# Kernel tuning notes

Hardware: AMD Instinct MI355X
Metric: run time of the kernel (lower is better)

The kernel has to match this reference:

```python
import jax, jax.numpy as jnp
import numpy as np

N = 262144      # active coordinates
M = 131072      # rulebook entries per kernel offset
C_IN = 64
C_OUT = 64


def setup_inputs() -> dict:
    key = jax.random.key(0)
    k1, k2, k3, k4 = jax.random.split(key, 4)
    coords = jax.random.randint(k1, (N, 3), 0, 512, dtype=jnp.int64) if jax.config.jax_enable_x64 else jax.random.randint(k1, (N, 3), 0, 512, dtype=jnp.int32)
    feats = jax.random.normal(k2, (N, C_IN), dtype=jnp.float32)
    in_rows = jax.random.randint(k3, (9, M), 0, N, dtype=jnp.int32)
    out_rows = jax.random.randint(k4, (9, M), 0, N, dtype=jnp.int32)
    # weight init matches torch: randn * (1/sqrt(in_ch))
    weight = jax.random.normal(jax.random.fold_in(key, 5), (9, C_IN, C_OUT), dtype=jnp.float32) * (1.0 / C_IN ** 0.5)
    bias = jnp.zeros((C_OUT,), dtype=jnp.float32)
    return {"coords": coords, "feats": feats, "in_rows": in_rows,
            "out_rows": out_rows, "weight": weight, "bias": bias}


def reference(coords, feats, in_rows, out_rows, weight, bias):
    # Gather input features for all 9 kernel offsets: [9, M, C_in]
    gathered = feats[in_rows]
    # Per-offset GEMM: [9, M, C_out]
    prod = jnp.einsum('kmi,kio->kmo', gathered, weight)
    # Scatter-add into output rows
    out = jnp.zeros((feats.shape[0], weight.shape[2]), dtype=feats.dtype)
    out = out.at[out_rows.reshape(-1)].add(prod.reshape(-1, weight.shape[2]))
    out = out + bias
    return (coords, out)
```

## Files before the change

### kernel.cpp

```cpp
#include <hip/hip_runtime.h>
#include <hip/hip_bf16.h>

#define NPTS 262144
#define MRB  131072
#define KOFF 9
#define NENT (KOFF * MRB)

typedef __attribute__((ext_vector_type(8))) short short8;
typedef __attribute__((ext_vector_type(4))) short short4v;
typedef __attribute__((ext_vector_type(4))) float f32x4;

__device__ __forceinline__ short f2bf(float f) {
    __hip_bfloat16 h = __float2bfloat16(f);
    return __builtin_bit_cast(short, h);
}
__device__ __forceinline__ float bf2f(unsigned short u) {
    unsigned int x = ((unsigned int)u) << 16;
    return __builtin_bit_cast(float, x);
}
__device__ __forceinline__ void atomic_add_f32(float* p, float v) {
    __hip_atomic_fetch_add(p, v, __ATOMIC_RELAXED, __HIP_MEMORY_SCOPE_AGENT);
}

#define PROD_OFF   0ull
#define POS_OFF    150994944ull
#define START_OFF  155713536ull
#define CURSOR_OFF 156762368ull
#define COUNTS_OFF 157810944ull
#define BSUM_OFF   158859520ull
#define WS_NEED    158860544ull


__global__ __launch_bounds__(256) void init_fast(const int* __restrict__ coords,
                                                 float* __restrict__ out,
                                                 int* __restrict__ counts) {
    const int i = blockIdx.x * 256 + threadIdx.x;
    const int nc4 = (NPTS * 3) / 4;
    if (i < nc4) {
        int4 c = ((const int4*)coords)[i];
        float4 f;
        f.x = (float)c.x; f.y = (float)c.y; f.z = (float)c.z; f.w = (float)c.w;
        ((float4*)out)[i] = f;
    } else {
        int j = i - nc4;
        ((int4*)counts)[j] = make_int4(0, 0, 0, 0);
    }
}

__global__ __launch_bounds__(256) void hist_kernel(const int* __restrict__ out_rows,
                                                   int* __restrict__ counts) {
    const int e = blockIdx.x * 256 + threadIdx.x;
    atomicAdd(&counts[out_rows[e]], 1);
}

__global__ __launch_bounds__(1024) void scan_blocks(const int* __restrict__ counts,
                                                    int* __restrict__ start,
                                                    int* __restrict__ bsum) {
    __shared__ int lds[1024];
    const int tid = threadIdx.x;
    const int gid = blockIdx.x * 1024 + tid;
    int v = counts[gid];
    lds[tid] = v;
    __syncthreads();
#pragma unroll
    for (int off = 1; off < 1024; off <<= 1) {
        int t = (tid >= off) ? lds[tid - off] : 0;
        __syncthreads();
        lds[tid] += t;
        __syncthreads();
    }
    start[gid] = lds[tid] - v;
    if (tid == 1023) bsum[blockIdx.x] = lds[tid];
}

__global__ __launch_bounds__(256) void scan_bsum(int* __restrict__ bsum) {
    __shared__ int lds[256];
    const int tid = threadIdx.x;
    int v = bsum[tid];
    lds[tid] = v;
    __syncthreads();
#pragma unroll
    for (int off = 1; off < 256; off <<= 1) {
        int t = (tid >= off) ? lds[tid - off] : 0;
        __syncthreads();
        lds[tid] += t;
        __syncthreads();
    }
    bsum[tid] = lds[tid] - v;
}

__global__ __launch_bounds__(1024) void add_offsets(int* __restrict__ start,
                                                    const int* __restrict__ bsum,
                                                    int* __restrict__ cursor) {
    const int gid = blockIdx.x * 1024 + threadIdx.x;
    int s = start[gid] + bsum[blockIdx.x];
    start[gid] = s;
    cursor[gid] = s;
    if (gid == 0) start[NPTS] = NENT;
}

__global__ __launch_bounds__(256) void fill_pos(const int* __restrict__ out_rows,
                                                int* __restrict__ cursor,
                                                int* __restrict__ pos) {
    const int e = blockIdx.x * 256 + threadIdx.x;
    pos[e] = atomicAdd(&cursor[out_rows[e]], 1);
}

__global__ __launch_bounds__(256) void conv_prod(const float* __restrict__ feats,
                                                 const int*   __restrict__ in_rows,
                                                 const float* __restrict__ weight,
                                                 const int*   __restrict__ pos,
                                                 short*       __restrict__ prod) {
    const int lane = threadIdx.x & 63;
    const int wv   = threadIdx.x >> 6;
    const int lrow = lane & 15;
    const int lhi  = lane >> 4;
    const int BPK  = MRB / 64;
    const int k    = blockIdx.x / BPK;
    const int mb   = (blockIdx.x % BPK) * 64 + wv * 16;

    const float* Wk = weight + k * 64 * 64;
    short8 wfrag[2][4];
#pragma unroll
    for (int kk = 0; kk < 2; ++kk)
#pragma unroll
        for (int mt = 0; mt < 4; ++mt)
#pragma unroll
            for (int j = 0; j < 8; ++j)
                wfrag[kk][mt][j] = f2bf(Wk[(kk * 32 + lhi * 8 + j) * 64 + mt * 16 + lrow]);

    const int e    = k * MRB + mb + lrow;
    const int arow = in_rows[e];
    const float* ap = feats + (long)arow * 64 + lhi * 8;

    f32x4 acc[4] = {};
#pragma unroll
    for (int kk = 0; kk < 2; ++kk) {
        float4 f0 = *(const float4*)(ap + kk * 32);
        float4 f1 = *(const float4*)(ap + kk * 32 + 4);
        short8 ffrag;
        ffrag[0] = f2bf(f0.x); ffrag[1] = f2bf(f0.y);
        ffrag[2] = f2bf(f0.z); ffrag[3] = f2bf(f0.w);
        ffrag[4] = f2bf(f1.x); ffrag[5] = f2bf(f1.y);
        ffrag[6] = f2bf(f1.z); ffrag[7] = f2bf(f1.w);
#pragma unroll
        for (int mt = 0; mt < 4; ++mt)
            acc[mt] = __builtin_amdgcn_mfma_f32_16x16x32_bf16(wfrag[kk][mt], ffrag, acc[mt], 0, 0, 0);
    }

    const int p = pos[e];
    short* pp = prod + (size_t)p * 64 + lhi * 4;
#pragma unroll
    for (int mt = 0; mt < 4; ++mt) {
        short4v s;
        s[0] = f2bf(acc[mt][0]); s[1] = f2bf(acc[mt][1]);
        s[2] = f2bf(acc[mt][2]); s[3] = f2bf(acc[mt][3]);
        *(short4v*)(pp + mt * 16) = s;
    }
}

__global__ __launch_bounds__(256) void reduce_out(const short* __restrict__ prod,
                                                  const int*   __restrict__ start,
                                                  const float* __restrict__ bias,
                                                  float*       __restrict__ out) {
    const int lane = threadIdx.x & 63;
    const int wid  = (blockIdx.x * 256 + threadIdx.x) >> 6;
    const int nw   = (gridDim.x * 256) >> 6;
    const float b  = bias[lane];
    for (int r = wid; r < NPTS; r += nw) {
        const int s0 = start[r], s1 = start[r + 1];
        float acc = 0.f;
        const unsigned short* p = (const unsigned short*)prod + (size_t)s0 * 64 + lane;
        for (int s = s0; s < s1; ++s, p += 64)
            acc += bf2f(*p);
        out[(size_t)r * 64 + lane] = acc + b;
    }
}

__global__ __launch_bounds__(256) void init_full(const int* __restrict__ coords,
                                                 const float* __restrict__ bias,
                                                 float* __restrict__ out) {
    const int tid = blockIdx.x * blockDim.x + threadIdx.x;
    const int nc4 = (NPTS * 3) / 4;
    const int nf4 = (NPTS * 64) / 4;
    for (int i = tid; i < nc4 + nf4; i += gridDim.x * blockDim.x) {
        if (i < nc4) {
            int4 c = ((const int4*)coords)[i];
            float4 f;
            f.x = (float)c.x; f.y = (float)c.y; f.z = (float)c.z; f.w = (float)c.w;
            ((float4*)out)[i] = f;
        } else {
            int j = i - nc4;
            float4 b = ((const float4*)bias)[j & 15];
            ((float4*)(out + (size_t)NPTS * 3))[j] = b;
        }
    }
}

__global__ __launch_bounds__(256) void conv_atomic(const float* __restrict__ feats,
                                                   const int*   __restrict__ in_rows,
                                                   const int*   __restrict__ out_rows,
                                                   const float* __restrict__ weight,
                                                   float*       __restrict__ out) {
    const int lane = threadIdx.x & 63;
    const int wv   = threadIdx.x >> 6;
    const int lrow = lane & 15;
    const int lhi  = lane >> 4;
    const int BPK  = MRB / 64;
    const int k    = blockIdx.x / BPK;
    const int mb   = (blockIdx.x % BPK) * 64 + wv * 16;

    const float* Wk = weight + k * 64 * 64;
    short8 bfrag[2][4];
#pragma unroll
    for (int kk = 0; kk < 2; ++kk)
#pragma unroll
        for (int nt = 0; nt < 4; ++nt)
#pragma unroll
            for (int j = 0; j < 8; ++j)
                bfrag[kk][nt][j] = f2bf(Wk[(kk * 32 + lhi * 8 + j) * 64 + nt * 16 + lrow]);

    const int arow = in_rows[k * MRB + mb + lrow];
    const float* ap = feats + (long)arow * 64 + lhi * 8;

    f32x4 acc[4] = {};
#pragma unroll
    for (int kk = 0; kk < 2; ++kk) {
        float4 f0 = *(const float4*)(ap + kk * 32);
        float4 f1 = *(const float4*)(ap + kk * 32 + 4);
        short8 afrag;
        afrag[0] = f2bf(f0.x); afrag[1] = f2bf(f0.y);
        afrag[2] = f2bf(f0.z); afrag[3] = f2bf(f0.w);
        afrag[4] = f2bf(f1.x); afrag[5] = f2bf(f1.y);
        afrag[6] = f2bf(f1.z); afrag[7] = f2bf(f1.w);
#pragma unroll
        for (int nt = 0; nt < 4; ++nt)
            acc[nt] = __builtin_amdgcn_mfma_f32_16x16x32_bf16(afrag, bfrag[kk][nt], acc[nt], 0, 0, 0);
    }

    const int ob = k * MRB + mb + lhi * 4;
#pragma unroll
    for (int r = 0; r < 4; ++r) {
        const int orow = out_rows[ob + r];
        float* op = out + (long)orow * 64 + lrow;
#pragma unroll
        for (int nt = 0; nt < 4; ++nt)
            atomic_add_f32(op + nt * 16, acc[nt][r]);
    }
}

extern "C" void kernel_launch(void* const* d_in, const int* in_sizes, int n_in,
                              void* d_out, int out_size, void* d_ws, size_t ws_size,
                              hipStream_t stream) {
    const int*   coords   = (const int*)  d_in[0];
    const float* feats    = (const float*)d_in[1];
    const int*   in_rows  = (const int*)  d_in[2];
    const int*   out_rows = (const int*)  d_in[3];
    const float* weight   = (const float*)d_in[4];
    const float* bias     = (const float*)d_in[5];
    float* out      = (float*)d_out;
    float* out_feat = out + (size_t)NPTS * 3;

    if (ws_size >= WS_NEED) {
        char* ws = (char*)d_ws;
        short* prod  = (short*)(ws + PROD_OFF);
        int* pos     = (int*)(ws + POS_OFF);
        int* start   = (int*)(ws + START_OFF);
        int* cursor  = (int*)(ws + CURSOR_OFF);
        int* counts  = (int*)(ws + COUNTS_OFF);
        int* bsum    = (int*)(ws + BSUM_OFF);

        hipLaunchKernelGGL(init_fast,   dim3(1024), dim3(256),  0, stream, coords, out, counts);
        hipLaunchKernelGGL(hist_kernel, dim3(NENT / 256), dim3(256), 0, stream, out_rows, counts);
        hipLaunchKernelGGL(scan_blocks, dim3(NPTS / 1024), dim3(1024), 0, stream, counts, start, bsum);
        hipLaunchKernelGGL(scan_bsum,   dim3(1),    dim3(256),  0, stream, bsum);
        hipLaunchKernelGGL(add_offsets, dim3(NPTS / 1024), dim3(1024), 0, stream, start, bsum, cursor);
        hipLaunchKernelGGL(fill_pos,    dim3(NENT / 256), dim3(256), 0, stream, out_rows, cursor, pos);
        hipLaunchKernelGGL(conv_prod,   dim3(KOFF * (MRB / 64)), dim3(256), 0, stream,
                           feats, in_rows, weight, pos, prod);
        hipLaunchKernelGGL(reduce_out,  dim3(2048), dim3(256),  0, stream, prod, start, bias, out_feat);
    } else {
        hipLaunchKernelGGL(init_full,  dim3(2048), dim3(256), 0, stream, coords, bias, out);
        hipLaunchKernelGGL(conv_atomic, dim3(KOFF * (MRB / 64)), dim3(256), 0, stream,
                           feats, in_rows, out_rows, weight, out_feat);
    }
}
```

Measured before the change: 439.8 us.

## Pre-convert feats and weights to bf16, write prod in entry order, gather via index

A prep kernel now converts feats to bf16 and pre-swizzles weights into MFMA fragment layout once, so conv_prod reads half the gathered bytes and skips per-block weight conversion. conv_prod writes products contiguously by entry instead of scattering to sorted positions, and fill_idx records a sorted index list instead. reduce_out then gathers products through that index with four rows in flight per wave and reduces with shuffles. The cost is an extra feats pass, extra workspace, and indirect, less coalesced reads in the reduction.

```diff
diff --git a/kernel.cpp b/kernel.cpp
--- a/kernel.cpp
+++ b/kernel.cpp
@@ -22,28 +22,56 @@
     __hip_atomic_fetch_add(p, v, __ATOMIC_RELAXED, __HIP_MEMORY_SCOPE_AGENT);
 }
 
-#define PROD_OFF   0ull
-#define POS_OFF    150994944ull
-#define START_OFF  155713536ull
-#define CURSOR_OFF 156762368ull
-#define COUNTS_OFF 157810944ull
-#define BSUM_OFF   158859520ull
-#define WS_NEED    158860544ull
-
-
-__global__ __launch_bounds__(256) void init_fast(const int* __restrict__ coords,
-                                                 float* __restrict__ out,
-                                                 int* __restrict__ counts) {
-    const int i = blockIdx.x * 256 + threadIdx.x;
-    const int nc4 = (NPTS * 3) / 4;
-    if (i < nc4) {
-        int4 c = ((const int4*)coords)[i];
-        float4 f;
-        f.x = (float)c.x; f.y = (float)c.y; f.z = (float)c.z; f.w = (float)c.w;
-        ((float4*)out)[i] = f;
-    } else {
-        int j = i - nc4;
-        ((int4*)counts)[j] = make_int4(0, 0, 0, 0);
+#define FB_OFF     0ull
+#define WBF_OFF    33554432ull
+#define PROD_OFF   33628160ull
+#define IDX_OFF    184623104ull
+#define START_OFF  189341696ull
+#define CURSOR_OFF 190390528ull
+#define COUNTS_OFF 191439104ull
+#define BSUM_OFF   192487680ull
+#define WS_NEED    192488704ull
+
+
+__global__ __launch_bounds__(256) void prep(const int*   __restrict__ coords,
+                                            const float* __restrict__ feats,
+                                            const float* __restrict__ weight,
+                                            float* __restrict__ out,
+                                            int*   __restrict__ counts,
+                                            short* __restrict__ fb,
+                                            short* __restrict__ wbf) {
+    const int T0 = (NPTS * 3) / 4;
+    const int T1 = T0 + NPTS / 4;
+    const int T2 = T1 + NPTS * 16;
+    const int T3 = T2 + (KOFF * 8 * 64);
+    const int stride = gridDim.x * 256;
+    for (int i = blockIdx.x * 256 + threadIdx.x; i < T3; i += stride) {
+        if (i < T0) {
+            int4 c = ((const int4*)coords)[i];
+            float4 f;
+            f.x = (float)c.x; f.y = (float)c.y; f.z = (float)c.z; f.w = (float)c.w;
+            ((float4*)out)[i] = f;
+        } else if (i < T1) {
+            ((int4*)counts)[i - T0] = make_int4(0, 0, 0, 0);
+        } else if (i < T2) {
+            int j = i - T1;
+            float4 f = ((const float4*)feats)[j];
+            short4v s;
+            s[0] = f2bf(f.x); s[1] = f2bf(f.y); s[2] = f2bf(f.z); s[3] = f2bf(f.w);
+            ((short4v*)fb)[j] = s;
+        } else {
+            int w    = i - T2;
+            int lane = w & 63;
+            int g    = w >> 6;
+            int mt   = g & 3, kk = (g >> 2) & 1, k = g >> 3;
+            int lhi  = lane >> 4, lrow = lane & 15;
+            const float* Wk = weight + k * 64 * 64;
+            short8 v;
+#pragma unroll
+            for (int j = 0; j < 8; ++j)
+                v[j] = f2bf(Wk[(kk * 32 + lhi * 8 + j) * 64 + mt * 16 + lrow]);
+            ((short8*)wbf)[g * 64 + lane] = v;
+        }
     }
 }
 
@@ -99,17 +127,16 @@
     if (gid == 0) start[NPTS] = NENT;
 }
 
-__global__ __launch_bounds__(256) void fill_pos(const int* __restrict__ out_rows,
+__global__ __launch_bounds__(256) void fill_idx(const int* __restrict__ out_rows,
                                                 int* __restrict__ cursor,
-                                                int* __restrict__ pos) {
+                                                int* __restrict__ idx) {
     const int e = blockIdx.x * 256 + threadIdx.x;
-    pos[e] = atomicAdd(&cursor[out_rows[e]], 1);
-}
-
-__global__ __launch_bounds__(256) void conv_prod(const float* __restrict__ feats,
+    idx[atomicAdd(&cursor[out_rows[e]], 1)] = e;
+}
+
+__global__ __launch_bounds__(256) void conv_prod(const short* __restrict__ fb,
                                                  const int*   __restrict__ in_rows,
-                                                 const float* __restrict__ weight,
-                                                 const int*   __restrict__ pos,
+                                                 const short* __restrict__ wbf,
                                                  short*       __restrict__ prod) {
     const int lane = threadIdx.x & 63;
     const int wv   = threadIdx.x >> 6;
@@ -119,37 +146,27 @@
     const int k    = blockIdx.x / BPK;
     const int mb   = (blockIdx.x % BPK) * 64 + wv * 16;
 
-    const float* Wk = weight + k * 64 * 64;
     short8 wfrag[2][4];
 #pragma unroll
     for (int kk = 0; kk < 2; ++kk)
 #pragma unroll
         for (int mt = 0; mt < 4; ++mt)
-#pragma unroll
-            for (int j = 0; j < 8; ++j)
-                wfrag[kk][mt][j] = f2bf(Wk[(kk * 32 + lhi * 8 + j) * 64 + mt * 16 + lrow]);
+            wfrag[kk][mt] = ((const short8*)wbf)[(k * 8 + kk * 4 + mt) * 64 + lane];
 
     const int e    = k * MRB + mb + lrow;
     const int arow = in_rows[e];
-    const float* ap = feats + (long)arow * 64 + lhi * 8;
+    const short* ap = fb + (size_t)arow * 64 + lhi * 8;
 
     f32x4 acc[4] = {};
 #pragma unroll
     for (int kk = 0; kk < 2; ++kk) {
-        float4 f0 = *(const float4*)(ap + kk * 32);
-        float4 f1 = *(const float4*)(ap + kk * 32 + 4);
-        short8 ffrag;
-        ffrag[0] = f2bf(f0.x); ffrag[1] = f2bf(f0.y);
-        ffrag[2] = f2bf(f0.z); ffrag[3] = f2bf(f0.w);
-        ffrag[4] = f2bf(f1.x); ffrag[5] = f2bf(f1.y);
-        ffrag[6] = f2bf(f1.z); ffrag[7] = f2bf(f1.w);
+        short8 ffrag = *(const short8*)(ap + kk * 32);
 #pragma unroll
         for (int mt = 0; mt < 4; ++mt)
             acc[mt] = __builtin_amdgcn_mfma_f32_16x16x32_bf16(wfrag[kk][mt], ffrag, acc[mt], 0, 0, 0);
     }
 
-    const int p = pos[e];
-    short* pp = prod + (size_t)p * 64 + lhi * 4;
+    short* pp = prod + (size_t)e * 64 + lhi * 4;
 #pragma unroll
     for (int mt = 0; mt < 4; ++mt) {
         short4v s;
@@ -160,20 +177,39 @@
 }
 
 __global__ __launch_bounds__(256) void reduce_out(const short* __restrict__ prod,
+                                                  const int*   __restrict__ idx,
                                                   const int*   __restrict__ start,
                                                   const float* __restrict__ bias,
                                                   float*       __restrict__ out) {
-    const int lane = threadIdx.x & 63;
-    const int wid  = (blockIdx.x * 256 + threadIdx.x) >> 6;
-    const int nw   = (gridDim.x * 256) >> 6;
-    const float b  = bias[lane];
+    const int lane  = threadIdx.x & 63;
+    const int lrow  = lane & 15;
+    const int phase = lane >> 4;
+    const int wid   = (blockIdx.x * 256 + threadIdx.x) >> 6;
+    const int nw    = (gridDim.x * 256) >> 6;
+    const float4 b4 = ((const float4*)bias)[lrow];
+
     for (int r = wid; r < NPTS; r += nw) {
         const int s0 = start[r], s1 = start[r + 1];
-        float acc = 0.f;
-        const unsigned short* p = (const unsigned short*)prod + (size_t)s0 * 64 + lane;
-        for (int s = s0; s < s1; ++s, p += 64)
-            acc += bf2f(*p);
-        out[(size_t)r * 64 + lane] = acc + b;
+        f32x4 a = {};
+        for (int s = s0 + phase; s < s1; s += 4) {
+            const int e = idx[s];
+            short4v v = *(const short4v*)(prod + (size_t)e * 64 + lrow * 4);
+            a[0] += bf2f((unsigned short)v[0]);
+            a[1] += bf2f((unsigned short)v[1]);
+            a[2] += bf2f((unsigned short)v[2]);
+            a[3] += bf2f((unsigned short)v[3]);
+        }
+#pragma unroll
+        for (int c = 0; c < 4; ++c) {
+            a[c] += __shfl_xor(a[c], 16);
+            a[c] += __shfl_xor(a[c], 32);
+        }
+        if (lane < 16) {
+            float4 o;
+            o.x = a[0] + b4.x; o.y = a[1] + b4.y;
+            o.z = a[2] + b4.z; o.w = a[3] + b4.w;
+            ((float4*)(out + (size_t)r * 64))[lrow] = o;
+        }
     }
 }
 
@@ -263,24 +299,28 @@
 
     if (ws_size >= WS_NEED) {
         char* ws = (char*)d_ws;
+        short* fb    = (short*)(ws + FB_OFF);
+        short* wbf   = (short*)(ws + WBF_OFF);
         short* prod  = (short*)(ws + PROD_OFF);
-        int* pos     = (int*)(ws + POS_OFF);
+        int* idx     = (int*)(ws + IDX_OFF);
         int* start   = (int*)(ws + START_OFF);
         int* cursor  = (int*)(ws + CURSOR_OFF);
         int* counts  = (int*)(ws + COUNTS_OFF);
         int* bsum    = (int*)(ws + BSUM_OFF);
 
-        hipLaunchKernelGGL(init_fast,   dim3(1024), dim3(256),  0, stream, coords, out, counts);
+        hipLaunchKernelGGL(prep,        dim3(2048), dim3(256), 0, stream,
+                           coords, feats, weight, out, counts, fb, wbf);
         hipLaunchKernelGGL(hist_kernel, dim3(NENT / 256), dim3(256), 0, stream, out_rows, counts);
         hipLaunchKernelGGL(scan_blocks, dim3(NPTS / 1024), dim3(1024), 0, stream, counts, start, bsum);
-        hipLaunchKernelGGL(scan_bsum,   dim3(1),    dim3(256),  0, stream, bsum);
+        hipLaunchKernelGGL(scan_bsum,   dim3(1), dim3(256), 0, stream, bsum);
         hipLaunchKernelGGL(add_offsets, dim3(NPTS / 1024), dim3(1024), 0, stream, start, bsum, cursor);
-        hipLaunchKernelGGL(fill_pos,    dim3(NENT / 256), dim3(256), 0, stream, out_rows, cursor, pos);
+        hipLaunchKernelGGL(fill_idx,    dim3(NENT / 256), dim3(256), 0, stream, out_rows, cursor, idx);
         hipLaunchKernelGGL(conv_prod,   dim3(KOFF * (MRB / 64)), dim3(256), 0, stream,
-                           feats, in_rows, weight, pos, prod);
-        hipLaunchKernelGGL(reduce_out,  dim3(2048), dim3(256),  0, stream, prod, start, bias, out_feat);
+                           fb, in_rows, wbf, prod);
+        hipLaunchKernelGGL(reduce_out,  dim3(2048), dim3(256), 0, stream,
+                           prod, idx, start, bias, out_feat);
     } else {
-        hipLaunchKernelGGL(init_full,  dim3(2048), dim3(256), 0, stream, coords, bias, out);
+        hipLaunchKernelGGL(init_full,   dim3(2048), dim3(256), 0, stream, coords, bias, out);
         hipLaunchKernelGGL(conv_atomic, dim3(KOFF * (MRB / 64)), dim3(256), 0, stream,
                            feats, in_rows, out_rows, weight, out_feat);
     }
```

After: 416.3 us. 5.3% less time.
